# Kernel optimization log

Hardware: AMD Instinct MI355X
Metric: run time of the kernel (lower is better)

The kernel has to match this reference:

```python
import jax, jax.numpy as jnp
import numpy as np

TOP_P = 0.95        # sample() default topp
TEMPERATURE = 0.8   # token_temperature
NEG_INF = float('-inf')


def setup_inputs() -> dict:
    key = jax.random.key(0)
    k1, k2 = jax.random.split(key)
    B, V = 8192, 2048  # batch rows x speech-unit vocab
    logits = jax.random.normal(k1, (B, V), dtype=jnp.float32) * 4.0
    # uniform noise for Gumbel-max multinomial sampling (open interval)
    u = jax.random.uniform(k2, (B, V), dtype=jnp.float32, minval=1e-6, maxval=1.0 - 1e-6)
    return {"logits": logits, "u": u}


def _top_p_filter(logits, p):
    # descending sort (matches torch.sort(descending=True))
    order = jnp.argsort(-logits, axis=-1)                      # [B, V]
    sorted_logits = jnp.take_along_axis(logits, order, axis=-1)
    cum = jnp.cumsum(jax.nn.softmax(sorted_logits, axis=-1), axis=-1)
    remove = cum > p
    # shift right by one so the first token above the threshold is kept
    remove = jnp.concatenate(
        [jnp.zeros_like(remove[..., :1]), remove[..., :-1]], axis=-1)
    # scatter mask back to unsorted order via inverse permutation
    inv = jnp.argsort(order, axis=-1)
    remove_unsorted = jnp.take_along_axis(remove, inv, axis=-1)
    return jnp.where(remove_unsorted, NEG_INF, logits)


def reference(logits, u):
    scaled = logits / TEMPERATURE
    filtered = _top_p_filter(scaled, TOP_P)                    # [B, V]
    probs = jax.nn.softmax(filtered, axis=-1)                  # [B, V]
    # multinomial(probs, 1) == Gumbel-max over filtered logits
    gumbel = -jnp.log(-jnp.log(u))
    sampled = jnp.argmax(filtered + gumbel, axis=-1, keepdims=True)  # [B, 1]
    return sampled, probs
```

## Files before the change

kernel.cpp:

```cpp
#include <hip/hip_runtime.h>
#include <math.h>

#define VOCAB 2048
#define TPB   256
#define NBINS 64
#define BIN_SCALE 6.0f

typedef float vf4 __attribute__((ext_vector_type(4)));

__global__ __launch_bounds__(TPB, 8) void sampler_kernel(
    const float* __restrict__ logits,
    const float* __restrict__ uni,
    float* __restrict__ out_idx,
    float* __restrict__ out_probs)
{
    const int row  = blockIdx.x;
    const int t    = threadIdx.x;
    const int lane = t & 63;
    const int wid  = t >> 6;

    __shared__ float  s_bins[NBINS];
    __shared__ float  s_wf[4];
    __shared__ double s_wd[4];
    __shared__ float  s_wk[4];
    __shared__ unsigned long long s_key[4];
    __shared__ double s_S, s_cumBefore;
    __shared__ int    s_bstar, s_cnt, s_cnt2;
    __shared__ float  s_cv[VOCAB];
    __shared__ float  s_ce[VOCAB];

    const float* lrow = logits    + (size_t)row * VOCAB;
    const float* urow = uni       + (size_t)row * VOCAB;
    float*       prow = out_probs + (size_t)row * VOCAB;

    if (t < NBINS) s_bins[t] = 0.0f;
    if (t == 0)    { s_cnt = 0; s_cnt2 = 0; }

    const vf4 a0 = *(const vf4*)(lrow + 4 * t);
    const vf4 a1 = *(const vf4*)(lrow + VOCAB / 2 + 4 * t);
    float s[8] = {a0.x * 1.25f, a0.y * 1.25f, a0.z * 1.25f, a0.w * 1.25f,
                  a1.x * 1.25f, a1.y * 1.25f, a1.z * 1.25f, a1.w * 1.25f};

    float lm = s[0];
    #pragma unroll
    for (int j = 1; j < 8; j++) lm = fmaxf(lm, s[j]);
    #pragma unroll
    for (int off = 32; off; off >>= 1) lm = fmaxf(lm, __shfl_down(lm, off));
    if (lane == 0) s_wf[wid] = lm;
    __syncthreads();
    const float m = fmaxf(fmaxf(s_wf[0], s_wf[1]), fmaxf(s_wf[2], s_wf[3]));

    float e[8];
    int   bin[8];
    float psum = 0.0f;
    #pragma unroll
    for (int j = 0; j < 8; j++) {
        e[j] = __expf(s[j] - m);
        psum += e[j];
        bin[j] = (int)((m - s[j]) * BIN_SCALE);
        if (bin[j] < NBINS) atomicAdd(&s_bins[bin[j]], e[j]);
    }
    double dp = (double)psum;
    #pragma unroll
    for (int off = 32; off; off >>= 1) dp += __shfl_down(dp, off);
    if (lane == 0) s_wd[wid] = dp;
    __syncthreads();

    if (wid == 0) {
        double S  = s_wd[0] + s_wd[1] + s_wd[2] + s_wd[3];
        float  bf = s_bins[lane];
        double c  = (double)bf;
        #pragma unroll
        for (int d = 1; d < 64; d <<= 1) {
            double o = __shfl_up(c, d);
            if (lane >= d) c += o;
        }
        double pS = 0.95 * S;
        unsigned long long ball = __ballot(c > pS);
        int bstar = ball ? (__ffsll(ball) - 1) : (NBINS - 1);
        double excl = c - (double)bf;
        double cumB = __shfl(excl, bstar);
        if (lane == 0) { s_S = S; s_bstar = bstar; s_cumBefore = cumB; }
    }
    __syncthreads();
    const double pS        = 0.95 * s_S;
    const int    bstar     = s_bstar;
    const double cumBefore = s_cumBefore;

    #pragma unroll
    for (int j = 0; j < 8; j++) {
        if (bin[j] == bstar) {
            int pos = atomicAdd(&s_cnt, 1);
            s_cv[pos] = s[j];
            s_ce[pos] = e[j];
        }
    }
    __syncthreads();
    const int cnt = s_cnt;

    unsigned keptMask = 0;
    float    kpsum    = 0.0f;
    #pragma unroll
    for (int j = 0; j < 8; j++) {
        bool kept;
        if (bin[j] < bstar)      kept = true;
        else if (bin[j] > bstar) kept = false;
        else {
            float part = 0.0f;
            for (int i = 0; i < cnt; i++)
                if (s_cv[i] > s[j]) part += s_ce[i];
            kept = (cumBefore + (double)part) <= pS;
        }
        if (kept) { keptMask |= (1u << j); kpsum += e[j]; }
    }
    #pragma unroll
    for (int off = 32; off; off >>= 1) kpsum += __shfl_down(kpsum, off);
    if (lane == 0) s_wk[wid] = kpsum;
    __syncthreads();
    const float SK    = s_wk[0] + s_wk[1] + s_wk[2] + s_wk[3];
    const float invSK = 1.0f / SK;

    vf4 p0, p1;
    p0.x = (keptMask & 0x01) ? e[0] * invSK : 0.0f;
    p0.y = (keptMask & 0x02) ? e[1] * invSK : 0.0f;
    p0.z = (keptMask & 0x04) ? e[2] * invSK : 0.0f;
    p0.w = (keptMask & 0x08) ? e[3] * invSK : 0.0f;
    p1.x = (keptMask & 0x10) ? e[4] * invSK : 0.0f;
    p1.y = (keptMask & 0x20) ? e[5] * invSK : 0.0f;
    p1.z = (keptMask & 0x40) ? e[6] * invSK : 0.0f;
    p1.w = (keptMask & 0x80) ? e[7] * invSK : 0.0f;
    __builtin_nontemporal_store(p0, (vf4*)(prow + 4 * t));
    __builtin_nontemporal_store(p1, (vf4*)(prow + VOCAB / 2 + 4 * t));

    #pragma unroll
    for (int j = 0; j < 8; j++) {
        if ((keptMask >> j) & 1u) {
            int idx = (j < 4) ? (4 * t + j) : (VOCAB / 2 + 4 * t + (j - 4));
            int pos = atomicAdd(&s_cnt2, 1);
            s_cv[pos] = s[j];
            s_ce[pos] = __int_as_float(idx);
        }
    }
    __syncthreads();
    const int k = s_cnt2;

    unsigned long long key = 0ull;
    for (int i = t; i < k; i += TPB) {
        float sv  = s_cv[i];
        int   idx = __float_as_int(s_ce[i]);
        float uv  = urow[idx];
        float g   = -logf(-logf(uv));
        float z   = sv + g;
        unsigned zb = __float_as_uint(z);
        zb = (zb & 0x80000000u) ? ~zb : (zb | 0x80000000u);
        unsigned long long kk =
            ((unsigned long long)zb << 32) | (unsigned)(VOCAB - 1 - idx);
        key = (kk > key) ? kk : key;
    }
    #pragma unroll
    for (int off = 32; off; off >>= 1) {
        unsigned long long ok = __shfl_down(key, off);
        key = (ok > key) ? ok : key;
    }
    if (lane == 0) s_key[wid] = key;
    __syncthreads();
    if (t == 0) {
        unsigned long long k0 = s_key[0];
        #pragma unroll
        for (int w = 1; w < 4; w++) k0 = (s_key[w] > k0) ? s_key[w] : k0;
        out_idx[row] = (float)(VOCAB - 1 - (int)(k0 & 0xFFFFFFFFu));
    }
}

extern "C" void kernel_launch(void* const* d_in, const int* in_sizes, int n_in,
                              void* d_out, int out_size, void* d_ws, size_t ws_size,
                              hipStream_t stream) {
    const float* logits = (const float*)d_in[0];
    const float* u      = (const float*)d_in[1];
    const int B = in_sizes[0] / VOCAB;
    float* out_idx   = (float*)d_out;
    float* out_probs = (float*)d_out + B;
    sampler_kernel<<<B, TPB, 0, stream>>>(logits, u, out_idx, out_probs);
}
```

Measured before the change: 164.5 us.

## Remove barriers by redundant per-wave scan and boundary-bin sum, preload noise

Every wave now runs the bin prefix scan itself, which removes one block barrier. Each thread recomputes the kept sum of the boundary bin redundantly, which replaces a block reduction and its barrier. The uniform noise is loaded with coalesced vector loads up front instead of gathered later. The final argmax skips the cross-wave barrier when 64 or fewer tokens are kept. In exchange, shared buffers are capped in size with an overflow path, and the redundant O(cnt^2) loop over the boundary bin adds ALU work per thread. The noise read also becomes a full row read, no longer limited to the kept tokens.

```diff
diff --git a/kernel.cpp b/kernel.cpp
--- a/kernel.cpp
+++ b/kernel.cpp
@@ -5,8 +5,16 @@
 #define TPB   256
 #define NBINS 64
 #define BIN_SCALE 6.0f
+#define BCAP  512
+#define KCAP  512
 
 typedef float vf4 __attribute__((ext_vector_type(4)));
+
+__device__ __forceinline__ unsigned long long pack_key(float z, int idx) {
+    unsigned zb = __float_as_uint(z);
+    zb = (zb & 0x80000000u) ? ~zb : (zb | 0x80000000u);
+    return ((unsigned long long)zb << 32) | (unsigned)(VOCAB - 1 - idx);
+}
 
 __global__ __launch_bounds__(TPB, 8) void sampler_kernel(
     const float* __restrict__ logits,
@@ -22,24 +30,28 @@
     __shared__ float  s_bins[NBINS];
     __shared__ float  s_wf[4];
     __shared__ double s_wd[4];
-    __shared__ float  s_wk[4];
     __shared__ unsigned long long s_key[4];
-    __shared__ double s_S, s_cumBefore;
-    __shared__ int    s_bstar, s_cnt, s_cnt2;
-    __shared__ float  s_cv[VOCAB];
-    __shared__ float  s_ce[VOCAB];
+    __shared__ int    s_cnt, s_cnt2;
+    __shared__ float  s_cv[BCAP];
+    __shared__ float  s_ce[BCAP];
+    __shared__ float  s_kv[KCAP];
+    __shared__ float  s_ku[KCAP];
+    __shared__ int    s_ki[KCAP];
 
     const float* lrow = logits    + (size_t)row * VOCAB;
     const float* urow = uni       + (size_t)row * VOCAB;
     float*       prow = out_probs + (size_t)row * VOCAB;
 
     if (t < NBINS) s_bins[t] = 0.0f;
-    if (t == 0)    { s_cnt = 0; s_cnt2 = 0; }
+    if (t == 0) { s_cnt = 0; s_cnt2 = 0; }
 
     const vf4 a0 = *(const vf4*)(lrow + 4 * t);
     const vf4 a1 = *(const vf4*)(lrow + VOCAB / 2 + 4 * t);
-    float s[8] = {a0.x * 1.25f, a0.y * 1.25f, a0.z * 1.25f, a0.w * 1.25f,
-                  a1.x * 1.25f, a1.y * 1.25f, a1.z * 1.25f, a1.w * 1.25f};
+    const vf4 u0 = *(const vf4*)(urow + 4 * t);
+    const vf4 u1 = *(const vf4*)(urow + VOCAB / 2 + 4 * t);
+    float s[8]  = {a0.x * 1.25f, a0.y * 1.25f, a0.z * 1.25f, a0.w * 1.25f,
+                   a1.x * 1.25f, a1.y * 1.25f, a1.z * 1.25f, a1.w * 1.25f};
+    float uu[8] = {u0.x, u0.y, u0.z, u0.w, u1.x, u1.y, u1.z, u1.w};
 
     float lm = s[0];
     #pragma unroll
@@ -51,14 +63,13 @@
     const float m = fmaxf(fmaxf(s_wf[0], s_wf[1]), fmaxf(s_wf[2], s_wf[3]));
 
     float e[8];
-    int   bin[8];
     float psum = 0.0f;
     #pragma unroll
     for (int j = 0; j < 8; j++) {
         e[j] = __expf(s[j] - m);
         psum += e[j];
-        bin[j] = (int)((m - s[j]) * BIN_SCALE);
-        if (bin[j] < NBINS) atomicAdd(&s_bins[bin[j]], e[j]);
+        int b = (int)((m - s[j]) * BIN_SCALE);
+        if (b < NBINS) atomicAdd(&s_bins[b], e[j]);
     }
     double dp = (double)psum;
     #pragma unroll
@@ -66,59 +77,54 @@
     if (lane == 0) s_wd[wid] = dp;
     __syncthreads();
 
-    if (wid == 0) {
-        double S  = s_wd[0] + s_wd[1] + s_wd[2] + s_wd[3];
-        float  bf = s_bins[lane];
-        double c  = (double)bf;
-        #pragma unroll
-        for (int d = 1; d < 64; d <<= 1) {
-            double o = __shfl_up(c, d);
-            if (lane >= d) c += o;
-        }
-        double pS = 0.95 * S;
-        unsigned long long ball = __ballot(c > pS);
-        int bstar = ball ? (__ffsll(ball) - 1) : (NBINS - 1);
-        double excl = c - (double)bf;
-        double cumB = __shfl(excl, bstar);
-        if (lane == 0) { s_S = S; s_bstar = bstar; s_cumBefore = cumB; }
-    }
-    __syncthreads();
-    const double pS        = 0.95 * s_S;
-    const int    bstar     = s_bstar;
-    const double cumBefore = s_cumBefore;
-
-    #pragma unroll
-    for (int j = 0; j < 8; j++) {
-        if (bin[j] == bstar) {
+    const double S  = s_wd[0] + s_wd[1] + s_wd[2] + s_wd[3];
+    const double pS = 0.95 * S;
+    const float  bf = s_bins[lane];
+    double c = (double)bf;
+    #pragma unroll
+    for (int d = 1; d < 64; d <<= 1) {
+        double o = __shfl_up(c, d);
+        if (lane >= d) c += o;
+    }
+    unsigned long long ball = __ballot(c > pS);
+    const int    bstar     = ball ? (__ffsll(ball) - 1) : (NBINS - 1);
+    const double cumBefore = __shfl(c - (double)bf, bstar);
+
+    #pragma unroll
+    for (int j = 0; j < 8; j++) {
+        int b = (int)((m - s[j]) * BIN_SCALE);
+        if (b == bstar) {
             int pos = atomicAdd(&s_cnt, 1);
-            s_cv[pos] = s[j];
-            s_ce[pos] = e[j];
-        }
-    }
-    __syncthreads();
-    const int cnt = s_cnt;
+            if (pos < BCAP) { s_cv[pos] = s[j]; s_ce[pos] = e[j]; }
+        }
+    }
+    __syncthreads();
+    const int cnt = min(s_cnt, BCAP);
+
+    float SKb = 0.0f;
+    for (int i = 0; i < cnt; i++) {
+        float vi = s_cv[i], part = 0.0f;
+        for (int jj = 0; jj < cnt; jj++)
+            part += (s_cv[jj] > vi) ? s_ce[jj] : 0.0f;
+        if (cumBefore + (double)part <= pS) SKb += s_ce[i];
+    }
+    const float invSK = 1.0f / (float)(cumBefore + (double)SKb);
 
     unsigned keptMask = 0;
-    float    kpsum    = 0.0f;
-    #pragma unroll
-    for (int j = 0; j < 8; j++) {
+    #pragma unroll
+    for (int j = 0; j < 8; j++) {
+        int  b = (int)((m - s[j]) * BIN_SCALE);
         bool kept;
-        if (bin[j] < bstar)      kept = true;
-        else if (bin[j] > bstar) kept = false;
+        if (b < bstar)      kept = true;
+        else if (b > bstar) kept = false;
         else {
             float part = 0.0f;
             for (int i = 0; i < cnt; i++)
-                if (s_cv[i] > s[j]) part += s_ce[i];
+                part += (s_cv[i] > s[j]) ? s_ce[i] : 0.0f;
             kept = (cumBefore + (double)part) <= pS;
         }
-        if (kept) { keptMask |= (1u << j); kpsum += e[j]; }
-    }
-    #pragma unroll
-    for (int off = 32; off; off >>= 1) kpsum += __shfl_down(kpsum, off);
-    if (lane == 0) s_wk[wid] = kpsum;
-    __syncthreads();
-    const float SK    = s_wk[0] + s_wk[1] + s_wk[2] + s_wk[3];
-    const float invSK = 1.0f / SK;
+        if (kept) keptMask |= (1u << j);
+    }
 
     vf4 p0, p1;
     p0.x = (keptMask & 0x01) ? e[0] * invSK : 0.0f;
@@ -132,43 +138,55 @@
     __builtin_nontemporal_store(p0, (vf4*)(prow + 4 * t));
     __builtin_nontemporal_store(p1, (vf4*)(prow + VOCAB / 2 + 4 * t));
 
+    unsigned long long ovKey = 0ull;
     #pragma unroll
     for (int j = 0; j < 8; j++) {
         if ((keptMask >> j) & 1u) {
             int idx = (j < 4) ? (4 * t + j) : (VOCAB / 2 + 4 * t + (j - 4));
             int pos = atomicAdd(&s_cnt2, 1);
-            s_cv[pos] = s[j];
-            s_ce[pos] = __int_as_float(idx);
-        }
-    }
-    __syncthreads();
-    const int k = s_cnt2;
-
-    unsigned long long key = 0ull;
-    for (int i = t; i < k; i += TPB) {
-        float sv  = s_cv[i];
-        int   idx = __float_as_int(s_ce[i]);
-        float uv  = urow[idx];
-        float g   = -logf(-logf(uv));
-        float z   = sv + g;
-        unsigned zb = __float_as_uint(z);
-        zb = (zb & 0x80000000u) ? ~zb : (zb | 0x80000000u);
-        unsigned long long kk =
-            ((unsigned long long)zb << 32) | (unsigned)(VOCAB - 1 - idx);
+            if (pos < KCAP) { s_kv[pos] = s[j]; s_ku[pos] = uu[j]; s_ki[pos] = idx; }
+            else {
+                float z = s[j] + (-logf(-logf(uu[j])));
+                unsigned long long kk = pack_key(z, idx);
+                ovKey = (kk > ovKey) ? kk : ovKey;
+            }
+        }
+    }
+    __syncthreads();
+    const int k  = s_cnt2;
+    const int kl = min(k, KCAP);
+
+    unsigned long long key = ovKey;
+    for (int i = t; i < kl; i += TPB) {
+        float z = s_kv[i] + (-logf(-logf(s_ku[i])));
+        unsigned long long kk = pack_key(z, s_ki[i]);
         key = (kk > key) ? kk : key;
     }
-    #pragma unroll
-    for (int off = 32; off; off >>= 1) {
-        unsigned long long ok = __shfl_down(key, off);
-        key = (ok > key) ? ok : key;
-    }
-    if (lane == 0) s_key[wid] = key;
-    __syncthreads();
-    if (t == 0) {
-        unsigned long long k0 = s_key[0];
+
+    if (k <= 64) {
+        if (wid == 0) {
+            #pragma unroll
+            for (int off = 32; off; off >>= 1) {
+                unsigned long long ok = __shfl_down(key, off);
+                key = (ok > key) ? ok : key;
+            }
+            if (lane == 0)
+                out_idx[row] = (float)(VOCAB - 1 - (int)(key & 0xFFFFFFFFu));
+        }
+    } else {
         #pragma unroll
-        for (int w = 1; w < 4; w++) k0 = (s_key[w] > k0) ? s_key[w] : k0;
-        out_idx[row] = (float)(VOCAB - 1 - (int)(k0 & 0xFFFFFFFFu));
+        for (int off = 32; off; off >>= 1) {
+            unsigned long long ok = __shfl_down(key, off);
+            key = (ok > key) ? ok : key;
+        }
+        if (lane == 0) s_key[wid] = key;
+        __syncthreads();
+        if (t == 0) {
+            unsigned long long k0 = s_key[0];
+            #pragma unroll
+            for (int w = 1; w < 4; w++) k0 = (s_key[w] > k0) ? s_key[w] : k0;
+            out_idx[row] = (float)(VOCAB - 1 - (int)(k0 & 0xFFFFFFFFu));
+        }
     }
 }
 
```

Result: slower. 184.2 us (+12.0%).
